# Kernel tuning notes

Hardware: AMD Instinct MI355X
Metric: run time of the kernel (lower is better)

Reference implementation:

```python
import jax, jax.numpy as jnp
import numpy as np

HID = 256


def _mlp(h, ws, bs):
    # 4-layer MLP: tanh x3, sigmoid output (matches nn.Sequential in torch code)
    h = jnp.tanh(h @ ws[0] + bs[0])
    h = jnp.tanh(h @ ws[1] + bs[1])
    h = jnp.tanh(h @ ws[2] + bs[2])
    return jax.nn.sigmoid(h @ ws[3] + bs[3])


def setup_inputs() -> dict:
    key = jax.random.key(0)
    N, K, DE = 100000, 32, 8
    IN1 = K * DE          # 256
    MID = 5
    IN2 = K * MID         # 160
    E = N * K
    ks = jax.random.split(key, 20)
    x = jax.random.normal(ks[0], (N, DE), dtype=jnp.float32)
    edge_index = jax.random.randint(ks[1], (2, E), 0, N, dtype=jnp.int64)
    edge_attr = jax.random.normal(ks[2], (E, DE), dtype=jnp.float32)

    def lin(k, fan_in, fan_out):
        kw, kb = jax.random.split(k)
        lim = 1.0 / np.sqrt(fan_in)
        w = jax.random.uniform(kw, (fan_in, fan_out), jnp.float32, -lim, lim)
        b = jax.random.uniform(kb, (fan_out,), jnp.float32, -lim, lim)
        return w, b

    dims1 = [(IN1, HID), (HID, HID), (HID, HID), (HID, MID)]
    dims2 = [(IN2, HID), (HID, HID), (HID, HID), (HID, 1)]
    inp = {"x": x, "edge_index": edge_index, "edge_attr": edge_attr}
    for i, (fi, fo) in enumerate(dims1):
        w, b = lin(ks[3 + i], fi, fo)
        inp[f"w1_{i}"], inp[f"b1_{i}"] = w, b
    for i, (fi, fo) in enumerate(dims2):
        w, b = lin(ks[10 + i], fi, fo)
        inp[f"w2_{i}"], inp[f"b2_{i}"] = w, b
    return inp


def reference(x, edge_index, edge_attr,
              w1_0, b1_0, w1_1, b1_1, w1_2, b1_2, w1_3, b1_3,
              w2_0, b2_0, w2_1, b2_1, w2_2, b2_2, w2_3, b2_3):
    K = 32
    IN1 = w1_0.shape[0]              # 256
    MID = w1_3.shape[1]              # 5
    # GNN1: message = edge_attr; aggregate reshapes to [N, IN1] then MLP -> [N, MID]
    out1 = _mlp(edge_attr.reshape(-1, IN1), (w1_0, w1_1, w1_2, w1_3), (b1_0, b1_1, b1_2, b1_3))
    # GNN2: message = x_j = out1[edge_index[1]] (flow='target_to_source')
    gathered = out1[edge_index[1]]                     # [E, MID] irregular gather
    out2 = _mlp(gathered.reshape(-1, K * MID), (w2_0, w2_1, w2_2, w2_3), (b2_0, b2_1, b2_2, b2_3))
    return out2[:, 0]                                  # squeeze dim 1 -> [N]
```

## Files before the change

kernel.cpp:

```cpp
#include <hip/hip_runtime.h>
#include <stdint.h>

typedef uint16_t u16;
typedef uint32_t u32;
typedef __attribute__((ext_vector_type(8)))  __bf16 bf16x8;
typedef __attribute__((ext_vector_type(16))) float  f32x16;

#define NROWS   100000
#define E_EDGES 3200000

#define HIDX(r, g) (((r) << 8) + ((((g) ^ ((r) & 31))) << 3))

#define MFMA(a, b, c) __builtin_amdgcn_mfma_f32_32x32x16_bf16((a), (b), (c), 0, 0, 0)

__device__ __forceinline__ u32 pk2(float a, float b) {
    u32 ua = __builtin_bit_cast(u32, a), ub = __builtin_bit_cast(u32, b);
    ua = (ua + 0x7FFFu + ((ua >> 16) & 1u)) >> 16;
    ub = (ub + 0x7FFFu + ((ub >> 16) & 1u)) >> 16;
    return ua | (ub << 16);
}
__device__ __forceinline__ float fast_tanh(float x) {
    float e = __builtin_amdgcn_exp2f(x * 2.885390081777927f);
    float r = __builtin_amdgcn_rcpf(e + 1.0f);
    return __builtin_fmaf(-2.0f, r, 1.0f);
}
__device__ __forceinline__ float fast_sigmoid(float x) {
    float e = __builtin_amdgcn_exp2f(x * -1.4426950408889634f);
    return __builtin_amdgcn_rcpf(1.0f + e);
}

__device__ __forceinline__ void dense256(u16* __restrict__ Hs, const u16* __restrict__ WB,
                                         const float* __restrict__ bias,
                                         int wave, int l31, int lh) {
    f32x16 acc[4];
#pragma unroll
    for (int i = 0; i < 4; ++i)
#pragma unroll
        for (int j = 0; j < 16; ++j) acc[i][j] = 0.0f;

    __syncthreads();

    const u16* wp = WB + (wave * 64 + l31) * 16 + lh * 8;
    bf16x8 w0 = *(const bf16x8*)(wp);
    bf16x8 w1 = *(const bf16x8*)(wp + 512);
    bf16x8 h0 = *(const bf16x8*)(Hs + HIDX(l31, lh));
    bf16x8 h1 = *(const bf16x8*)(Hs + HIDX(32 + l31, lh));

#pragma unroll
    for (int s = 0; s < 16; ++s) {
        bf16x8 nw0 = w0, nw1 = w1, nh0 = h0, nh1 = h1;
        if (s < 15) {
            const int ng = 2 * (s + 1) + lh;
            nw0 = *(const bf16x8*)(wp + (s + 1) * 4096);
            nw1 = *(const bf16x8*)(wp + (s + 1) * 4096 + 512);
            nh0 = *(const bf16x8*)(Hs + HIDX(l31, ng));
            nh1 = *(const bf16x8*)(Hs + HIDX(32 + l31, ng));
        }
        acc[0] = MFMA(w0, h0, acc[0]);
        acc[1] = MFMA(w0, h1, acc[1]);
        acc[2] = MFMA(w1, h0, acc[2]);
        acc[3] = MFMA(w1, h1, acc[3]);
        w0 = nw0; w1 = nw1; h0 = nh0; h1 = nh1;
    }
    __syncthreads();

#pragma unroll
    for (int i = 0; i < 2; ++i) {
        const int nt = wave * 2 + i;
#pragma unroll
        for (int rg = 0; rg < 4; ++rg) {
            const float4 bv = *(const float4*)(bias + nt * 32 + rg * 8 + lh * 4);
#pragma unroll
            for (int b = 0; b < 2; ++b) {
                const f32x16& A = acc[i * 2 + b];
                float x0 = fast_tanh(A[rg * 4 + 0] + bv.x);
                float x1 = fast_tanh(A[rg * 4 + 1] + bv.y);
                float x2 = fast_tanh(A[rg * 4 + 2] + bv.z);
                float x3 = fast_tanh(A[rg * 4 + 3] + bv.w);
                const int r = b * 32 + l31;
                const int g = nt * 4 + rg;
                uint2 v; v.x = pk2(x0, x1); v.y = pk2(x2, x3);
                *(uint2*)(Hs + (r << 8) + (((g) ^ (r & 31)) << 3) + lh * 4) = v;
            }
        }
    }
}

__device__ __forceinline__ f32x16 final_dense(const u16* __restrict__ Hs,
                                              const u16* __restrict__ WBf,
                                              int wave, int l31, int lh) {
    __syncthreads();
    f32x16 acc;
#pragma unroll
    for (int j = 0; j < 16; ++j) acc[j] = 0.0f;
    if (wave < 2) {
        const u16* wp = WBf + l31 * 16 + lh * 8;
        bf16x8 w = *(const bf16x8*)(wp);
        bf16x8 h = *(const bf16x8*)(Hs + HIDX(wave * 32 + l31, lh));
#pragma unroll
        for (int s = 0; s < 16; ++s) {
            bf16x8 nw = w, nh = h;
            if (s < 15) {
                nw = *(const bf16x8*)(wp + (s + 1) * 512);
                nh = *(const bf16x8*)(Hs + HIDX(wave * 32 + l31, 2 * (s + 1) + lh));
            }
            acc = MFMA(w, h, acc);
            w = nw; h = nh;
        }
    }
    return acc;
}

__global__ __launch_bounds__(256, 4) void mlp1_kernel(
    const float* __restrict__ ea, const u16* __restrict__ WB1, const u16* __restrict__ WB13,
    const float* __restrict__ b0, const float* __restrict__ b1, const float* __restrict__ b2,
    const float* __restrict__ b3, u16* __restrict__ out1) {
    __shared__ u16 Hs[64 * 256];
    const int tid = threadIdx.x, wave = tid >> 6, lane = tid & 63, blk = blockIdx.x;
    const int l31 = lane & 31, lh = lane >> 5;

#pragma unroll
    for (int i = 0; i < 8; ++i) {
        const int li = i * 256 + tid;
        const int r = li >> 5, g = li & 31;
        const int rg_ = blk * 64 + r;
        uint4 v = {0u, 0u, 0u, 0u};
        if (rg_ < NROWS) {
            const float* p = ea + (size_t)rg_ * 256 + g * 8;
            float4 a0 = *(const float4*)p;
            float4 a1 = *(const float4*)(p + 4);
            v.x = pk2(a0.x, a0.y); v.y = pk2(a0.z, a0.w);
            v.z = pk2(a1.x, a1.y); v.w = pk2(a1.z, a1.w);
        }
        *(uint4*)(Hs + HIDX(r, g)) = v;
    }
    dense256(Hs, WB1,          b0, wave, l31, lh);
    dense256(Hs, WB1 + 65536,  b1, wave, l31, lh);
    dense256(Hs, WB1 + 131072, b2, wave, l31, lh);
    f32x16 acc = final_dense(Hs, WB13, wave, l31, lh);

    if (wave < 2) {
        const int row_g = blk * 64 + wave * 32 + l31;
        if (row_g < NROWS) {
            if (lh == 0) {
                float s0 = fast_sigmoid(acc[0] + b3[0]);
                float s1 = fast_sigmoid(acc[1] + b3[1]);
                float s2 = fast_sigmoid(acc[2] + b3[2]);
                float s3 = fast_sigmoid(acc[3] + b3[3]);
                uint2 v; v.x = pk2(s0, s1); v.y = pk2(s2, s3);
                *(uint2*)(out1 + (size_t)row_g * 8) = v;
            } else {
                float s4 = fast_sigmoid(acc[0] + b3[4]);
                uint2 v; v.x = pk2(s4, 0.0f); v.y = 0u;
                *(uint2*)(out1 + (size_t)row_g * 8 + 4) = v;
            }
        }
    }
}

__global__ __launch_bounds__(256, 4) void mlp2_kernel(
    const int* __restrict__ idx1, const u16* __restrict__ out1,
    const u16* __restrict__ WB2, const u16* __restrict__ WB23,
    const float* __restrict__ b0, const float* __restrict__ b1, const float* __restrict__ b2,
    const float* __restrict__ b3, float* __restrict__ out) {
    __shared__ u16 Hs[64 * 256];
    const int tid = threadIdx.x, wave = tid >> 6, lane = tid & 63, blk = blockIdx.x;
    const int l31 = lane & 31, lh = lane >> 5;

    int nodes[8];
#pragma unroll
    for (int i = 0; i < 8; ++i) {
        const long e = (long)blk * 2048 + i * 256 + tid;
        nodes[i] = (e < (long)E_EDGES) ? idx1[e] : -1;
    }
#pragma unroll
    for (int i = 0; i < 8; ++i) {
        const int li = i * 256 + tid;
        const int r = li >> 5, j = li & 31;
        uint4 v = {0u, 0u, 0u, 0u};
        if (nodes[i] >= 0) v = *(const uint4*)(out1 + (size_t)nodes[i] * 8);
        *(uint4*)(Hs + HIDX(r, j)) = v;
    }
    dense256(Hs, WB2,          b0, wave, l31, lh);
    dense256(Hs, WB2 + 65536,  b1, wave, l31, lh);
    dense256(Hs, WB2 + 131072, b2, wave, l31, lh);
    f32x16 acc = final_dense(Hs, WB23, wave, l31, lh);

    if (wave < 2) {
        const int row_g = blk * 64 + wave * 32 + l31;
        if (row_g < NROWS && lh == 0)
            out[row_g] = fast_sigmoid(acc[0] + b3[0]);
    }
}

__global__ void transform_kernel(
    const float* __restrict__ w10, const float* __restrict__ w11, const float* __restrict__ w12,
    const float* __restrict__ w13, const float* __restrict__ w20, const float* __restrict__ w21,
    const float* __restrict__ w22, const float* __restrict__ w23, u16* __restrict__ ws) {
    const int id = blockIdx.x * 256 + threadIdx.x;
    float val;
    if (id < 196608) {
        int layer = id >> 16, rem = id & 65535;
        int s = rem >> 12, n = (rem >> 4) & 255, kl = rem & 15;
        int k = s * 16 + kl;
        const float* w = layer == 0 ? w10 : (layer == 1 ? w11 : w12);
        val = w[k * 256 + n];
    } else if (id < 204800) {
        int rem = id - 196608;
        int s = rem >> 9, n = (rem >> 4) & 31, kl = rem & 15;
        int k = s * 16 + kl;
        val = (n < 5) ? w13[k * 5 + n] : 0.0f;
    } else if (id < 401408) {
        int rem = id - 204800;
        int layer = rem >> 16; rem &= 65535;
        int s = rem >> 12, n = (rem >> 4) & 255, kl = rem & 15;
        int k = s * 16 + kl;
        if (layer == 0) {
            int j = k >> 3, v = k & 7;
            val = (v < 5) ? w20[(j * 5 + v) * 256 + n] : 0.0f;
        } else {
            val = (layer == 1 ? w21 : w22)[k * 256 + n];
        }
    } else {
        int rem = id - 401408;
        int s = rem >> 9, n = (rem >> 4) & 31, kl = rem & 15;
        int k = s * 16 + kl;
        val = (n == 0) ? w23[k] : 0.0f;
    }
    u32 u = __builtin_bit_cast(u32, val);
    u = (u + 0x7FFFu + ((u >> 16) & 1u)) >> 16;
    ws[id] = (u16)u;
}

extern "C" void kernel_launch(void* const* d_in, const int* in_sizes, int n_in,
                              void* d_out, int out_size, void* d_ws, size_t ws_size,
                              hipStream_t stream) {
    const int*   ei  = (const int*)d_in[1];
    const float* ea  = (const float*)d_in[2];
    const float* w10 = (const float*)d_in[3];  const float* b10 = (const float*)d_in[4];
    const float* w11 = (const float*)d_in[5];  const float* b11 = (const float*)d_in[6];
    const float* w12 = (const float*)d_in[7];  const float* b12 = (const float*)d_in[8];
    const float* w13 = (const float*)d_in[9];  const float* b13 = (const float*)d_in[10];
    const float* w20 = (const float*)d_in[11]; const float* b20 = (const float*)d_in[12];
    const float* w21 = (const float*)d_in[13]; const float* b21 = (const float*)d_in[14];
    const float* w22 = (const float*)d_in[15]; const float* b22 = (const float*)d_in[16];
    const float* w23 = (const float*)d_in[17]; const float* b23 = (const float*)d_in[18];

    u16* ws   = (u16*)d_ws;
    u16* WB1  = ws;
    u16* WB13 = ws + 196608;
    u16* WB2  = ws + 204800;
    u16* WB23 = ws + 401408;
    u16* out1 = ws + 409600;

    hipLaunchKernelGGL(transform_kernel, dim3(1600), dim3(256), 0, stream,
                       w10, w11, w12, w13, w20, w21, w22, w23, ws);
    hipLaunchKernelGGL(mlp1_kernel, dim3(1563), dim3(256), 0, stream,
                       ea, WB1, WB13, b10, b11, b12, b13, out1);
    hipLaunchKernelGGL(mlp2_kernel, dim3(1563), dim3(256), 0, stream,
                       ei + E_EDGES, out1, WB2, WB23, b20, b21, b22, b23, (float*)d_out);
}
```

Baseline: 333.2 us.

## Persistent MLP kernels with register-resident weights and atomic tile scheduling

Both MLP kernels become persistent. They launch a fixed grid of 512-thread blocks, and each block pulls 64-row tiles from an atomic counter that the transform kernel resets on every call. Each of the 8 waves now owns 32 output columns and keeps its slice of the three hidden-layer weight matrices in registers for the whole run, instead of reloading weights from global memory for every tile. The aim is to remove repeated weight traffic and per-block launch overhead. The cost is heavy register pressure from 48 bf16x8 weight vectors per lane, which together with the launch bounds may force spills or limit occupancy.

Result: slower. 922.7 us (+177.0%).

```diff
diff --git a/kernel.cpp b/kernel.cpp
--- a/kernel.cpp
+++ b/kernel.cpp
@@ -8,6 +8,8 @@
 
 #define NROWS   100000
 #define E_EDGES 3200000
+#define NTILES  1563
+#define GRID    768
 
 #define HIDX(r, g) (((r) << 8) + ((((g) ^ ((r) & 31))) << 3))
 
@@ -29,59 +31,46 @@
     return __builtin_amdgcn_rcpf(1.0f + e);
 }
 
-__device__ __forceinline__ void dense256(u16* __restrict__ Hs, const u16* __restrict__ WB,
-                                         const float* __restrict__ bias,
-                                         int wave, int l31, int lh) {
-    f32x16 acc[4];
-#pragma unroll
-    for (int i = 0; i < 4; ++i)
-#pragma unroll
-        for (int j = 0; j < 16; ++j) acc[i][j] = 0.0f;
+__device__ __forceinline__ void dense64(u16* __restrict__ Hs, const bf16x8 (&W)[16],
+                                        const float* __restrict__ bias,
+                                        int wave, int l31, int lh) {
+    f32x16 acc0, acc1;
+#pragma unroll
+    for (int j = 0; j < 16; ++j) { acc0[j] = 0.0f; acc1[j] = 0.0f; }
 
     __syncthreads();
 
-    const u16* wp = WB + (wave * 64 + l31) * 16 + lh * 8;
-    bf16x8 w0 = *(const bf16x8*)(wp);
-    bf16x8 w1 = *(const bf16x8*)(wp + 512);
     bf16x8 h0 = *(const bf16x8*)(Hs + HIDX(l31, lh));
     bf16x8 h1 = *(const bf16x8*)(Hs + HIDX(32 + l31, lh));
 
 #pragma unroll
     for (int s = 0; s < 16; ++s) {
-        bf16x8 nw0 = w0, nw1 = w1, nh0 = h0, nh1 = h1;
+        bf16x8 nh0 = h0, nh1 = h1;
         if (s < 15) {
             const int ng = 2 * (s + 1) + lh;
-            nw0 = *(const bf16x8*)(wp + (s + 1) * 4096);
-            nw1 = *(const bf16x8*)(wp + (s + 1) * 4096 + 512);
             nh0 = *(const bf16x8*)(Hs + HIDX(l31, ng));
             nh1 = *(const bf16x8*)(Hs + HIDX(32 + l31, ng));
         }
-        acc[0] = MFMA(w0, h0, acc[0]);
-        acc[1] = MFMA(w0, h1, acc[1]);
-        acc[2] = MFMA(w1, h0, acc[2]);
-        acc[3] = MFMA(w1, h1, acc[3]);
-        w0 = nw0; w1 = nw1; h0 = nh0; h1 = nh1;
+        acc0 = MFMA(W[s], h0, acc0);
+        acc1 = MFMA(W[s], h1, acc1);
+        h0 = nh0; h1 = nh1;
     }
     __syncthreads();
 
 #pragma unroll
-    for (int i = 0; i < 2; ++i) {
-        const int nt = wave * 2 + i;
-#pragma unroll
-        for (int rg = 0; rg < 4; ++rg) {
-            const float4 bv = *(const float4*)(bias + nt * 32 + rg * 8 + lh * 4);
-#pragma unroll
-            for (int b = 0; b < 2; ++b) {
-                const f32x16& A = acc[i * 2 + b];
-                float x0 = fast_tanh(A[rg * 4 + 0] + bv.x);
-                float x1 = fast_tanh(A[rg * 4 + 1] + bv.y);
-                float x2 = fast_tanh(A[rg * 4 + 2] + bv.z);
-                float x3 = fast_tanh(A[rg * 4 + 3] + bv.w);
-                const int r = b * 32 + l31;
-                const int g = nt * 4 + rg;
-                uint2 v; v.x = pk2(x0, x1); v.y = pk2(x2, x3);
-                *(uint2*)(Hs + (r << 8) + (((g) ^ (r & 31)) << 3) + lh * 4) = v;
-            }
+    for (int rg = 0; rg < 4; ++rg) {
+        const float4 bv = *(const float4*)(bias + wave * 32 + rg * 8 + lh * 4);
+#pragma unroll
+        for (int b = 0; b < 2; ++b) {
+            const f32x16& A = b ? acc1 : acc0;
+            float x0 = fast_tanh(A[rg * 4 + 0] + bv.x);
+            float x1 = fast_tanh(A[rg * 4 + 1] + bv.y);
+            float x2 = fast_tanh(A[rg * 4 + 2] + bv.z);
+            float x3 = fast_tanh(A[rg * 4 + 3] + bv.w);
+            const int r = b * 32 + l31;
+            const int g = wave * 4 + rg;
+            uint2 v; v.x = pk2(x0, x1); v.y = pk2(x2, x3);
+            *(uint2*)(Hs + (r << 8) + (((g) ^ (r & 31)) << 3) + lh * 4) = v;
         }
     }
 }
@@ -111,85 +100,121 @@
     return acc;
 }
 
-__global__ __launch_bounds__(256, 4) void mlp1_kernel(
-    const float* __restrict__ ea, const u16* __restrict__ WB1, const u16* __restrict__ WB13,
+__global__ __launch_bounds__(512, 6) void mlp1_kernel(
+    const float* __restrict__ ea, const u16* __restrict__ WB1, const u16* __restrict__ WBf,
     const float* __restrict__ b0, const float* __restrict__ b1, const float* __restrict__ b2,
-    const float* __restrict__ b3, u16* __restrict__ out1) {
+    const float* __restrict__ b3, u16* __restrict__ out1, u32* __restrict__ cnt) {
     __shared__ u16 Hs[64 * 256];
-    const int tid = threadIdx.x, wave = tid >> 6, lane = tid & 63, blk = blockIdx.x;
+    __shared__ int tshare;
+    const int tid = threadIdx.x, wave = tid >> 6, lane = tid & 63;
     const int l31 = lane & 31, lh = lane >> 5;
 
-#pragma unroll
-    for (int i = 0; i < 8; ++i) {
-        const int li = i * 256 + tid;
-        const int r = li >> 5, g = li & 31;
-        const int rg_ = blk * 64 + r;
-        uint4 v = {0u, 0u, 0u, 0u};
-        if (rg_ < NROWS) {
-            const float* p = ea + (size_t)rg_ * 256 + g * 8;
-            float4 a0 = *(const float4*)p;
-            float4 a1 = *(const float4*)(p + 4);
-            v.x = pk2(a0.x, a0.y); v.y = pk2(a0.z, a0.w);
-            v.z = pk2(a1.x, a1.y); v.w = pk2(a1.z, a1.w);
-        }
-        *(uint4*)(Hs + HIDX(r, g)) = v;
-    }
-    dense256(Hs, WB1,          b0, wave, l31, lh);
-    dense256(Hs, WB1 + 65536,  b1, wave, l31, lh);
-    dense256(Hs, WB1 + 131072, b2, wave, l31, lh);
-    f32x16 acc = final_dense(Hs, WB13, wave, l31, lh);
-
-    if (wave < 2) {
-        const int row_g = blk * 64 + wave * 32 + l31;
-        if (row_g < NROWS) {
-            if (lh == 0) {
-                float s0 = fast_sigmoid(acc[0] + b3[0]);
-                float s1 = fast_sigmoid(acc[1] + b3[1]);
-                float s2 = fast_sigmoid(acc[2] + b3[2]);
-                float s3 = fast_sigmoid(acc[3] + b3[3]);
-                uint2 v; v.x = pk2(s0, s1); v.y = pk2(s2, s3);
-                *(uint2*)(out1 + (size_t)row_g * 8) = v;
-            } else {
-                float s4 = fast_sigmoid(acc[0] + b3[4]);
-                uint2 v; v.x = pk2(s4, 0.0f); v.y = 0u;
-                *(uint2*)(out1 + (size_t)row_g * 8 + 4) = v;
+    bf16x8 W0[16], W1[16], W2[16];
+    {
+        const u16* wp = WB1 + (wave * 32 + l31) * 16 + lh * 8;
+#pragma unroll
+        for (int s = 0; s < 16; ++s) {
+            W0[s] = *(const bf16x8*)(wp + s * 4096);
+            W1[s] = *(const bf16x8*)(wp + 65536 + s * 4096);
+            W2[s] = *(const bf16x8*)(wp + 131072 + s * 4096);
+        }
+    }
+
+    int t = blockIdx.x;
+    while (t < NTILES) {
+#pragma unroll
+        for (int i = 0; i < 4; ++i) {
+            const int li = i * 512 + tid;
+            const int r = li >> 5, g = li & 31;
+            const int rg_ = t * 64 + r;
+            uint4 v = {0u, 0u, 0u, 0u};
+            if (rg_ < NROWS) {
+                const float* p = ea + (size_t)rg_ * 256 + g * 8;
+                float4 a0 = *(const float4*)p;
+                float4 a1 = *(const float4*)(p + 4);
+                v.x = pk2(a0.x, a0.y); v.y = pk2(a0.z, a0.w);
+                v.z = pk2(a1.x, a1.y); v.w = pk2(a1.z, a1.w);
             }
-        }
-    }
-}
-
-__global__ __launch_bounds__(256, 4) void mlp2_kernel(
+            *(uint4*)(Hs + HIDX(r, g)) = v;
+        }
+        dense64(Hs, W0, b0, wave, l31, lh);
+        dense64(Hs, W1, b1, wave, l31, lh);
+        dense64(Hs, W2, b2, wave, l31, lh);
+        f32x16 acc = final_dense(Hs, WBf, wave, l31, lh);
+
+        if (wave < 2) {
+            const int row_g = t * 64 + wave * 32 + l31;
+            if (row_g < NROWS) {
+                if (lh == 0) {
+                    float s0 = fast_sigmoid(acc[0] + b3[0]);
+                    float s1 = fast_sigmoid(acc[1] + b3[1]);
+                    float s2 = fast_sigmoid(acc[2] + b3[2]);
+                    float s3 = fast_sigmoid(acc[3] + b3[3]);
+                    uint2 v; v.x = pk2(s0, s1); v.y = pk2(s2, s3);
+                    *(uint2*)(out1 + (size_t)row_g * 8) = v;
+                } else {
+                    float s4 = fast_sigmoid(acc[0] + b3[4]);
+                    uint2 v; v.x = pk2(s4, 0.0f); v.y = 0u;
+                    *(uint2*)(out1 + (size_t)row_g * 8 + 4) = v;
+                }
+            }
+        }
+        if (tid == 0) tshare = (int)atomicAdd(cnt, 1u);
+        __syncthreads();
+        t = tshare;
+    }
+}
+
+__global__ __launch_bounds__(512, 6) void mlp2_kernel(
     const int* __restrict__ idx1, const u16* __restrict__ out1,
-    const u16* __restrict__ WB2, const u16* __restrict__ WB23,
+    const u16* __restrict__ WB2, const u16* __restrict__ WBf,
     const float* __restrict__ b0, const float* __restrict__ b1, const float* __restrict__ b2,
-    const float* __restrict__ b3, float* __restrict__ out) {
+    const float* __restrict__ b3, float* __restrict__ out, u32* __restrict__ cnt) {
     __shared__ u16 Hs[64 * 256];
-    const int tid = threadIdx.x, wave = tid >> 6, lane = tid & 63, blk = blockIdx.x;
+    __shared__ int tshare;
+    const int tid = threadIdx.x, wave = tid >> 6, lane = tid & 63;
     const int l31 = lane & 31, lh = lane >> 5;
 
-    int nodes[8];
-#pragma unroll
-    for (int i = 0; i < 8; ++i) {
-        const long e = (long)blk * 2048 + i * 256 + tid;
-        nodes[i] = (e < (long)E_EDGES) ? idx1[e] : -1;
-    }
-#pragma unroll
-    for (int i = 0; i < 8; ++i) {
-        const int li = i * 256 + tid;
-        const int r = li >> 5, j = li & 31;
-        uint4 v = {0u, 0u, 0u, 0u};
-        if (nodes[i] >= 0) v = *(const uint4*)(out1 + (size_t)nodes[i] * 8);
-        *(uint4*)(Hs + HIDX(r, j)) = v;
-    }
-    dense256(Hs, WB2,          b0, wave, l31, lh);
-    dense256(Hs, WB2 + 65536,  b1, wave, l31, lh);
-    dense256(Hs, WB2 + 131072, b2, wave, l31, lh);
-    f32x16 acc = final_dense(Hs, WB23, wave, l31, lh);
-
-    if (wave < 2) {
-        const int row_g = blk * 64 + wave * 32 + l31;
-        if (row_g < NROWS && lh == 0)
-            out[row_g] = fast_sigmoid(acc[0] + b3[0]);
+    bf16x8 W0[16], W1[16], W2[16];
+    {
+        const u16* wp = WB2 + (wave * 32 + l31) * 16 + lh * 8;
+#pragma unroll
+        for (int s = 0; s < 16; ++s) {
+            W0[s] = *(const bf16x8*)(wp + s * 4096);
+            W1[s] = *(const bf16x8*)(wp + 65536 + s * 4096);
+            W2[s] = *(const bf16x8*)(wp + 131072 + s * 4096);
+        }
+    }
+
+    int t = blockIdx.x;
+    while (t < NTILES) {
+        int nodes[4];
+#pragma unroll
+        for (int i = 0; i < 4; ++i) {
+            const long e = (long)t * 2048 + i * 512 + tid;
+            nodes[i] = (e < (long)E_EDGES) ? idx1[e] : -1;
+        }
+#pragma unroll
+        for (int i = 0; i < 4; ++i) {
+            const int li = i * 512 + tid;
+            const int r = li >> 5, j = li & 31;
+            uint4 v = {0u, 0u, 0u, 0u};
+            if (nodes[i] >= 0) v = *(const uint4*)(out1 + (size_t)nodes[i] * 8);
+            *(uint4*)(Hs + HIDX(r, j)) = v;
+        }
+        dense64(Hs, W0, b0, wave, l31, lh);
+        dense64(Hs, W1, b1, wave, l31, lh);
+        dense64(Hs, W2, b2, wave, l31, lh);
+        f32x16 acc = final_dense(Hs, WBf, wave, l31, lh);
+
+        if (wave < 2) {
+            const int row_g = t * 64 + wave * 32 + l31;
+            if (row_g < NROWS && lh == 0)
+                out[row_g] = fast_sigmoid(acc[0] + b3[0]);
+        }
+        if (tid == 0) tshare = (int)atomicAdd(cnt, 1u);
+        __syncthreads();
+        t = tshare;
     }
 }
 
@@ -198,6 +223,10 @@
     const float* __restrict__ w13, const float* __restrict__ w20, const float* __restrict__ w21,
     const float* __restrict__ w22, const float* __restrict__ w23, u16* __restrict__ ws) {
     const int id = blockIdx.x * 256 + threadIdx.x;
+    if (id == 0) {
+        u32* cnt = (u32*)(ws + 409600);
+        cnt[0] = GRID; cnt[1] = GRID;
+    }
     float val;
     if (id < 196608) {
         int layer = id >> 16, rem = id & 65535;
@@ -251,12 +280,14 @@
     u16* WB13 = ws + 196608;
     u16* WB2  = ws + 204800;
     u16* WB23 = ws + 401408;
-    u16* out1 = ws + 409600;
+    u32* cnt  = (u32*)(ws + 409600);
+    u16* out1 = ws + 409608;
 
     hipLaunchKernelGGL(transform_kernel, dim3(1600), dim3(256), 0, stream,
                        w10, w11, w12, w13, w20, w21, w22, w23, ws);
-    hipLaunchKernelGGL(mlp1_kernel, dim3(1563), dim3(256), 0, stream,
-                       ea, WB1, WB13, b10, b11, b12, b13, out1);
-    hipLaunchKernelGGL(mlp2_kernel, dim3(1563), dim3(256), 0, stream,
-                       ei + E_EDGES, out1, WB2, WB23, b20, b21, b22, b23, (float*)d_out);
-}
+    hipLaunchKernelGGL(mlp1_kernel, dim3(GRID), dim3(512), 0, stream,
+                       ea, WB1, WB13, b10, b11, b12, b13, out1, cnt + 0);
+    hipLaunchKernelGGL(mlp2_kernel, dim3(GRID), dim3(512), 0, stream,
+                       ei + E_EDGES, out1, WB2, WB23, b20, b21, b22, b23, (float*)d_out,
+                       cnt + 1);
+}
```
